# Kernel tuning notes

Measured on AMD Instinct MI355X. Metric: run time of the kernel, lower is better.

Reference implementation:

```python
import jax, jax.numpy as jnp
import numpy as np

N_BASIS = 16


def _kan_layer(x, coeffs, centers):
    # x: [b, in], coeffs: [out, in, n], centers: [n]
    mu = jnp.mean(x, axis=0)
    sd = jnp.std(x, axis=0, ddof=1)  # torch.std is unbiased by default
    xn = jnp.clip((x - mu) / (sd + 1e-6), -3.0, 3.0)
    # Gaussian RBF expansion: [b, in, n]
    basis = jnp.exp(-((xn[..., None] - centers) ** 2) / 0.5)
    return jnp.einsum('bin,oin->bo', basis, coeffs)


def setup_inputs() -> dict:
    key = jax.random.key(0)
    ks = jax.random.split(key, 6)
    B, IN, H = 16384, 256, 512
    return {
        'x': jax.random.normal(ks[0], (B, IN), jnp.float32),
        'coeffs1': jax.random.normal(ks[1], (H, IN, N_BASIS), jnp.float32) * 0.1,
        'coeffs2': jax.random.normal(ks[2], (H, H, N_BASIS), jnp.float32) * 0.1,
        'coeffs3': jax.random.normal(ks[3], (1, H, N_BASIS), jnp.float32) * 0.1,
        'skip_w': jax.random.normal(ks[4], (1, IN), jnp.float32) * 0.05,
        'skip_b': jnp.zeros((1,), jnp.float32),
    }


def reference(x, coeffs1, coeffs2, coeffs3, skip_w, skip_b):
    centers = jnp.linspace(-2.0, 2.0, N_BASIS).astype(x.dtype)
    h = jnp.tanh(_kan_layer(x, coeffs1, centers))
    h = jnp.tanh(_kan_layer(h, coeffs2, centers))
    out = _kan_layer(h, coeffs3, centers)[:, 0]  # squeeze(-1)
    skip = (x @ skip_w.T + skip_b)[:, 0]
    return out + skip
```

## Files before the change

kernel.cpp:

```cpp
#include <hip/hip_runtime.h>
#include <cstdint>
#include <cstddef>

typedef __attribute__((ext_vector_type(8))) _Float16 half8;
typedef __attribute__((ext_vector_type(4))) _Float16 half4;
typedef __attribute__((ext_vector_type(2))) __fp16   fp16x2;
typedef __attribute__((ext_vector_type(4))) float    floatx4;

static constexpr int B_ROWS = 16384;
static constexpr int IN_DIM = 256;
static constexpr int H_DIM  = 512;
static constexpr int NB     = 16;

__device__ __forceinline__ float fast_tanh(float x) {
  float ax = fabsf(x);
  float e  = __expf(2.0f * ax);
  float t  = 1.0f - 2.0f / (e + 1.0f);
  return copysignf(t, x);
}

__device__ __forceinline__ void gld16(const void* g, void* l) {
  __builtin_amdgcn_global_load_lds(
      (const __attribute__((address_space(1))) unsigned int*)g,
      (__attribute__((address_space(3))) unsigned int*)l, 16, 0, 0);
}

__global__ __launch_bounds__(256) void prep_k(const float* __restrict__ c1, _Float16* __restrict__ d1, size_t n41,
                                              const float* __restrict__ c2, _Float16* __restrict__ d2, size_t n42,
                                              const float* __restrict__ X,
                                              float* __restrict__ ps, float* __restrict__ ps2) {
  const int bx = blockIdx.x;
  if (bx < 128) {
    int c     = (bx & 3) * 64 + (threadIdx.x & 63);
    int chunk = threadIdx.x >> 6;
    int seg   = bx >> 2;
    int r0    = seg * 512;
    double s = 0.0, s2 = 0.0;
    for (int r = r0 + chunk; r < r0 + 512; r += 4) {
      float v = X[(size_t)r * IN_DIM + c];
      s += v; s2 += (double)v * (double)v;
    }
    __shared__ float Ls[256], Ls2[256];
    Ls[threadIdx.x] = (float)s; Ls2[threadIdx.x] = (float)s2;
    __syncthreads();
    if (chunk == 0) {
      int cl = threadIdx.x;
      float a  = Ls[cl]  + Ls[cl + 64]  + Ls[cl + 128]  + Ls[cl + 192];
      float b  = Ls2[cl] + Ls2[cl + 64] + Ls2[cl + 128] + Ls2[cl + 192];
      ps [(size_t)seg * IN_DIM + c] = a;
      ps2[(size_t)seg * IN_DIM + c] = b;
    }
  } else {
    size_t tot = n41 + n42;
    int nb_blocks = gridDim.x - 128;
    for (size_t i = (size_t)(bx - 128) * 256 + threadIdx.x; i < tot;
         i += (size_t)nb_blocks * 256) {
      const float4* sp; half4* dp; size_t j;
      if (i < n41) { sp = (const float4*)c1; dp = (half4*)d1; j = i; }
      else         { sp = (const float4*)c2; dp = (half4*)d2; j = i - n41; }
      float4 v = sp[j];
      int nb = (int)((j << 2) & 15);
      half4 r;
      float e0 = -2.f + (float)(nb + 0) * (4.f / 15.f);
      float e1 = -2.f + (float)(nb + 1) * (4.f / 15.f);
      float e2 = -2.f + (float)(nb + 2) * (4.f / 15.f);
      float e3 = -2.f + (float)(nb + 3) * (4.f / 15.f);
      r[0] = (_Float16)(v.x * __expf(-2.f * e0 * e0));
      r[1] = (_Float16)(v.y * __expf(-2.f * e1 * e1));
      r[2] = (_Float16)(v.z * __expf(-2.f * e2 * e2));
      r[3] = (_Float16)(v.w * __expf(-2.f * e3 * e3));
      dp[j] = r;
    }
  }
}

__global__ void stats_final_k(const float* __restrict__ ps,
                              const float* __restrict__ ps2,
                              int segs, int cols, int rows,
                              float* __restrict__ nmi, float* __restrict__ isd,
                              float2* __restrict__ snpk) {
  int c = blockIdx.x * blockDim.x + threadIdx.x;
  if (c >= cols) return;
  double s = 0.0, s2 = 0.0;
  for (int g = 0; g < segs; g++) { s += ps[(size_t)g * cols + c]; s2 += ps2[(size_t)g * cols + c]; }
  double mean = s / rows;
  double var  = (s2 - s * s / rows) / (rows - 1);
  if (var < 0.0) var = 0.0;
  float sd = (float)sqrt(var);
  float iv = 1.0f / (sd + 1e-6f);
  float nm = -(float)mean * iv;
  isd[c] = iv;
  nmi[c] = nm;
  snpk[c] = make_float2(iv, nm);
}

__global__ __launch_bounds__(512, 4) void kan_gemm_fused(const float* __restrict__ X,
                                                         const float2* __restrict__ snpk,
                                                         const _Float16* __restrict__ Bm,
                                                         float* __restrict__ Hout,
                                                         float* __restrict__ psum,
                                                         float* __restrict__ psum2,
                                                         int C) {
  const int K = C << 4;
  const int steps = K >> 6;
  __shared__ __align__(16) unsigned char LDSB[81920];
  _Float16* const Asb = reinterpret_cast<_Float16*>(LDSB);
  _Float16* const Bsb = reinterpret_cast<_Float16*>(LDSB + 32768);
  const int tid  = threadIdx.x;
  const int w = tid >> 6, lane = tid & 63;
  const int wm = w & 1, wn = (w >> 1) & 1, ksw = w >> 2;
  const int lrow = lane & 15, quad = lane >> 4;
  const int row0 = blockIdx.x * 128;
  const int col0 = blockIdx.y * 128;
  const int kq = ksw * 4 + quad;

  const int s_row = tid >> 3;
  const int s_sl  = tid & 7;
  const int s_seg = s_sl ^ ((s_row >> 1) & 7);
  const _Float16* gB = Bm + (size_t)(col0 + s_row) * K + s_seg * 8;

  const int erow = tid & 127;
  const int eh   = tid >> 7;
  const float*  xp  = X    + (size_t)(row0 + erow) * C + eh;
  const float2* snp = snpk + eh;

  floatx4 acc[4][4] = {};

  auto expand_store = [&](float xr, float2 sn, int bufi) {
    float xn = fminf(fmaxf(fmaf(xr, sn.x, sn.y), -3.f), 3.f);
    float Wv = __expf(fmaf(-2.f, xn, -8.f) * xn);
    float g  = __expf((16.f / 15.f) * xn);
    float g2 = g * g, g4 = g2 * g2, g8 = g4 * g4;
    fp16x2 gg = __builtin_amdgcn_cvt_pkrtz(g2, g2);
    union { fp16x2 q[4]; half8 v8; } u0, u1;
    u0.q[0] = __builtin_amdgcn_cvt_pkrtz(Wv, Wv * g);
    u0.q[1] = u0.q[0] * gg;
    u0.q[2] = u0.q[1] * gg;
    u0.q[3] = u0.q[2] * gg;
    float W8 = Wv * g8;
    u1.q[0] = __builtin_amdgcn_cvt_pkrtz(W8, W8 * g);
    u1.q[1] = u1.q[0] * gg;
    u1.q[2] = u1.q[1] * gg;
    u1.q[3] = u1.q[2] * gg;
    int ks0 = 2 * eh;
    *(half8*)&Asb[(size_t)bufi * 8192 + (size_t)(ks0 * 128 + erow) * 8]       = u0.v8;
    *(half8*)&Asb[(size_t)bufi * 8192 + (size_t)((ks0 + 1) * 128 + erow) * 8] = u1.v8;
  };

  float  x0  = xp[0];
  float2 sn0 = snp[0];
  gld16(gB, &Bsb[(size_t)tid * 8]);
  gld16(gB + (size_t)64 * K, &Bsb[(size_t)(tid + 512) * 8]);
  __builtin_amdgcn_sched_barrier(0);
  gld16(gB + 64, &Bsb[8192 + (size_t)tid * 8]);
  gld16(gB + 64 + (size_t)64 * K, &Bsb[8192 + (size_t)(tid + 512) * 8]);
  __builtin_amdgcn_sched_barrier(0);
  float  xv = xp[4];
  float2 sv = snp[4];
  expand_store(x0, sn0, 0);
  asm volatile("s_waitcnt vmcnt(0)" ::: "memory");
  asm volatile("s_waitcnt lgkmcnt(0)" ::: "memory");
  __builtin_amdgcn_s_barrier();
  __builtin_amdgcn_sched_barrier(0);

  int bcur = 0;
  for (int k = 0; k < steps; k++) {
    const int abuf = k & 1;
    const bool more  = (k + 1 < steps);
    const bool more2 = (k + 2 < steps);
    const int b2 = (bcur == 0) ? 2 : bcur - 1;
    if (more2) {
      gld16(gB + (size_t)(k + 2) * 64, &Bsb[(size_t)b2 * 8192 + (size_t)tid * 8]);
      gld16(gB + (size_t)(k + 2) * 64 + (size_t)64 * K,
            &Bsb[(size_t)b2 * 8192 + (size_t)(tid + 512) * 8]);
      __builtin_amdgcn_sched_barrier(0);
    }
    half8 af[4], bf[4];
    auto read_frags = [&]() {
#pragma unroll
      for (int t = 0; t < 4; t++) {
        int arow = wm * 64 + t * 16 + lrow;
        af[t] = *(const half8*)&Asb[(size_t)abuf * 8192 + (size_t)(kq * 128 + arow) * 8];
      }
#pragma unroll
      for (int t = 0; t < 4; t++) {
        int brow = wn * 64 + t * 16 + lrow;
        int bchunk = brow * 8 + (kq ^ ((brow >> 1) & 7));
        bf[t] = *(const half8*)&Bsb[(size_t)bcur * 8192 + (size_t)bchunk * 8];
      }
    };
    auto do_expand = [&]() {
      if (more) {
        expand_store(xv, sv, abuf ^ 1);
        if (more2) {
          xv = xp[4 * (k + 2)];
          sv = snp[4 * (k + 2)];
        }
      }
    };
    if (ksw == 0) {
      read_frags();
      __builtin_amdgcn_s_setprio(1);
#pragma unroll
      for (int tm = 0; tm < 2; tm++)
#pragma unroll
        for (int tn = 0; tn < 4; tn++)
          acc[tm][tn] = __builtin_amdgcn_mfma_f32_16x16x32_f16(af[tm], bf[tn], acc[tm][tn], 0, 0, 0);
      __builtin_amdgcn_s_setprio(0);
      do_expand();
      __builtin_amdgcn_s_setprio(1);
#pragma unroll
      for (int tm = 2; tm < 4; tm++)
#pragma unroll
        for (int tn = 0; tn < 4; tn++)
          acc[tm][tn] = __builtin_amdgcn_mfma_f32_16x16x32_f16(af[tm], bf[tn], acc[tm][tn], 0, 0, 0);
      __builtin_amdgcn_s_setprio(0);
    } else {
      do_expand();
      read_frags();
      __builtin_amdgcn_s_setprio(1);
#pragma unroll
      for (int tm = 0; tm < 4; tm++)
#pragma unroll
        for (int tn = 0; tn < 4; tn++)
          acc[tm][tn] = __builtin_amdgcn_mfma_f32_16x16x32_f16(af[tm], bf[tn], acc[tm][tn], 0, 0, 0);
      __builtin_amdgcn_s_setprio(0);
    }
    asm volatile("s_waitcnt lgkmcnt(0)" ::: "memory");
    __builtin_amdgcn_s_barrier();
    __builtin_amdgcn_sched_barrier(0);
    bcur = (bcur == 2) ? 0 : bcur + 1;
  }

  float* MB = reinterpret_cast<float*>(LDSB);
  const int p = wm * 2 + wn;
  asm volatile("s_waitcnt vmcnt(0)" ::: "memory");
  if (ksw == 1) {
    float* dst = MB + (size_t)p * 4096;
#pragma unroll
    for (int tm = 0; tm < 4; tm++)
#pragma unroll
      for (int tn = 0; tn < 4; tn++)
        *(floatx4*)&dst[((tm * 4 + tn) * 64 + lane) * 4] = acc[tm][tn];
  }
  asm volatile("s_waitcnt lgkmcnt(0)" ::: "memory");
  __builtin_amdgcn_s_barrier();
  __builtin_amdgcn_sched_barrier(0);

  float* Rs1 = MB + 16384;
  float* Rs2 = Rs1 + 256;
  if (ksw == 0) {
    const float* src = MB + (size_t)p * 4096;
    float s1[4] = {0.f, 0.f, 0.f, 0.f}, s2v[4] = {0.f, 0.f, 0.f, 0.f};
#pragma unroll
    for (int tm = 0; tm < 4; tm++) {
#pragma unroll
      for (int tn = 0; tn < 4; tn++) {
        floatx4 other = *(const floatx4*)&src[((tm * 4 + tn) * 64 + lane) * 4];
        int gcol = col0 + wn * 64 + tn * 16 + lrow;
#pragma unroll
        for (int r = 0; r < 4; r++) {
          int grow = row0 + wm * 64 + tm * 16 + quad * 4 + r;
          float v = fast_tanh(acc[tm][tn][r] + other[r]);
          Hout[(size_t)grow * H_DIM + gcol] = v;
          s1[tn] += v; s2v[tn] += v * v;
        }
      }
    }
#pragma unroll
    for (int tn = 0; tn < 4; tn++) {
      s1[tn]  += __shfl_xor(s1[tn], 16);  s1[tn]  += __shfl_xor(s1[tn], 32);
      s2v[tn] += __shfl_xor(s2v[tn], 16); s2v[tn] += __shfl_xor(s2v[tn], 32);
    }
    if (quad == 0) {
#pragma unroll
      for (int tn = 0; tn < 4; tn++) {
        Rs1[wm * 128 + wn * 64 + tn * 16 + lrow] = s1[tn];
        Rs2[wm * 128 + wn * 64 + tn * 16 + lrow] = s2v[tn];
      }
    }
  }
  asm volatile("s_waitcnt lgkmcnt(0)" ::: "memory");
  __builtin_amdgcn_s_barrier();
  __builtin_amdgcn_sched_barrier(0);
  if (tid < 128) {
    psum [(size_t)blockIdx.x * H_DIM + col0 + tid] = Rs1[tid] + Rs1[128 + tid];
    psum2[(size_t)blockIdx.x * H_DIM + col0 + tid] = Rs2[tid] + Rs2[128 + tid];
  }
}

__global__ __launch_bounds__(256) void layer3_k(const float* __restrict__ H2,
                                                const float* __restrict__ nmi,
                                                const float* __restrict__ isd,
                                                const float* __restrict__ C3,
                                                const float* __restrict__ X,
                                                const float* __restrict__ SW,
                                                const float* __restrict__ SB,
                                                float* __restrict__ OUT) {
  int w = threadIdx.x >> 6, lane = threadIdx.x & 63;
  float Kn[NB];
#pragma unroll
  for (int n = 0; n < NB; n++) {
    float c = -2.f + (float)n * (4.f / 15.f);
    Kn[n] = __expf(-2.f * c * c);
  }
  float sb0 = SB[0];
  int row_base = blockIdx.x * 16 + w * 4;
  for (int r = 0; r < 4; r++) {
    int row = row_base + r;
    float s = 0.f;
#pragma unroll
    for (int j = 0; j < 8; j++) {
      int i = lane + 64 * j;
      float hv = H2[(size_t)row * H_DIM + i];
      float xn = fminf(fmaxf(fmaf(hv, isd[i], nmi[i]), -3.f), 3.f);
      float Wf = __expf(fmaf(-2.f, xn, -8.f) * xn);
      float gf = __expf((16.f / 15.f) * xn);
      const floatx4* cp = (const floatx4*)(C3 + (size_t)i * NB);
      floatx4 c0 = cp[0], c1 = cp[1], c2 = cp[2], c3 = cp[3];
      float p = Wf;
#pragma unroll
      for (int n = 0; n < 4; n++) { s += p * Kn[n]      * c0[n]; p *= gf; }
#pragma unroll
      for (int n = 0; n < 4; n++) { s += p * Kn[n + 4]  * c1[n]; p *= gf; }
#pragma unroll
      for (int n = 0; n < 4; n++) { s += p * Kn[n + 8]  * c2[n]; p *= gf; }
#pragma unroll
      for (int n = 0; n < 4; n++) { s += p * Kn[n + 12] * c3[n]; p *= gf; }
    }
#pragma unroll
    for (int j = 0; j < 4; j++) {
      int i = lane + 64 * j;
      s += X[(size_t)row * IN_DIM + i] * SW[i];
    }
#pragma unroll
    for (int off = 32; off > 0; off >>= 1) s += __shfl_down(s, off);
    if (lane == 0) OUT[row] = s + sb0;
  }
}

extern "C" void kernel_launch(void* const* d_in, const int* in_sizes, int n_in,
                              void* d_out, int out_size, void* d_ws, size_t ws_size,
                              hipStream_t stream) {
  const float* x  = (const float*)d_in[0];
  const float* c1 = (const float*)d_in[1];
  const float* c2 = (const float*)d_in[2];
  const float* c3 = (const float*)d_in[3];
  const float* sw = (const float*)d_in[4];
  const float* sb = (const float*)d_in[5];
  float* out = (float*)d_out;

  const int B = B_ROWS, IN = IN_DIM, H = H_DIM;

  char* ws = (char*)d_ws;
  size_t off = 0;
  auto alloc = [&](size_t bytes) -> void* {
    void* p = ws + off;
    off += (bytes + 255) & ~(size_t)255;
    return p;
  };
  _Float16* C1h = (_Float16*)alloc((size_t)H * IN * NB * 2);
  _Float16* C2h = (_Float16*)alloc((size_t)H * H  * NB * 2);
  float* H1 = (float*)alloc((size_t)B * H * 4);
  float* H2 = (float*)alloc((size_t)B * H * 4);
  float* ps  = (float*)alloc(128 * 512 * 4);
  float* ps2 = (float*)alloc(128 * 512 * 4);
  float* nmi = (float*)alloc(512 * 4);
  float* isd = (float*)alloc(512 * 4);
  float2* snpk = (float2*)alloc(512 * 8);

  prep_k<<<128 + 1024, 256, 0, stream>>>(c1, C1h, (size_t)H * IN * NB / 4,
                                         c2, C2h, (size_t)H * H * NB / 4,
                                         x, ps, ps2);
  stats_final_k<<<1, 256, 0, stream>>>(ps, ps2, 32, IN, B, nmi, isd, snpk);

  kan_gemm_fused<<<dim3(B / 128, 4), 512, 0, stream>>>(x, snpk, C1h, H1, ps, ps2, IN);
  stats_final_k<<<2, 256, 0, stream>>>(ps, ps2, 128, H, B, nmi, isd, snpk);

  kan_gemm_fused<<<dim3(B / 128, 4), 512, 0, stream>>>(H1, snpk, C2h, H2, ps, ps2, H);
  stats_final_k<<<2, 256, 0, stream>>>(ps, ps2, 128, H, B, nmi, isd, snpk);

  layer3_k<<<B / 16, 256, 0, stream>>>(H2, nmi, isd, c3, x, sw, sb, out);
}
```

Before: 440.1 us.

## Fuse all stages into one persistent kernel with software grid barriers

The seven separate launches (prep, three column-stat reductions, two GEMM layers, final layer) are merged into one persistent kernel of 512 blocks. The stages are separated by atomic grid barriers in global memory, and the column statistics are finalised in parallel with one column per block. The aim is to remove launch gaps and tail idle time between the dependent stages. In exchange, every block must be co-resident or the barriers deadlock, each barrier adds spin-wait cost, and the barrier counter needs a memset every call.

```diff
diff --git a/kernel.cpp b/kernel.cpp
--- a/kernel.cpp
+++ b/kernel.cpp
@@ -11,6 +11,7 @@
 static constexpr int IN_DIM = 256;
 static constexpr int H_DIM  = 512;
 static constexpr int NB     = 16;
+static constexpr int NBLK   = 512;
 
 __device__ __forceinline__ float fast_tanh(float x) {
   float ax = fabsf(x);
@@ -25,93 +26,59 @@
       (__attribute__((address_space(3))) unsigned int*)l, 16, 0, 0);
 }
 
-__global__ __launch_bounds__(256) void prep_k(const float* __restrict__ c1, _Float16* __restrict__ d1, size_t n41,
-                                              const float* __restrict__ c2, _Float16* __restrict__ d2, size_t n42,
-                                              const float* __restrict__ X,
-                                              float* __restrict__ ps, float* __restrict__ ps2) {
-  const int bx = blockIdx.x;
-  if (bx < 128) {
-    int c     = (bx & 3) * 64 + (threadIdx.x & 63);
-    int chunk = threadIdx.x >> 6;
-    int seg   = bx >> 2;
-    int r0    = seg * 512;
+__device__ __forceinline__ void grid_barrier(unsigned long long* bar, int idx) {
+  __syncthreads();
+  if (threadIdx.x == 0) {
+    __threadfence();
+    __hip_atomic_fetch_add(&bar[idx], 1ull, __ATOMIC_RELEASE, __HIP_MEMORY_SCOPE_AGENT);
+    while (__hip_atomic_load(&bar[idx], __ATOMIC_ACQUIRE, __HIP_MEMORY_SCOPE_AGENT)
+           < (unsigned long long)NBLK) {
+      __builtin_amdgcn_s_sleep(2);
+    }
+    __threadfence();
+  }
+  __syncthreads();
+}
+
+__device__ __forceinline__ void col_stats(const float* ps, const float* ps2,
+                                          int segs, int C, float2* snpk,
+                                          int b, int tid, double* Lred) {
+  if (b < C) {
     double s = 0.0, s2 = 0.0;
-    for (int r = r0 + chunk; r < r0 + 512; r += 4) {
-      float v = X[(size_t)r * IN_DIM + c];
-      s += v; s2 += (double)v * (double)v;
-    }
-    __shared__ float Ls[256], Ls2[256];
-    Ls[threadIdx.x] = (float)s; Ls2[threadIdx.x] = (float)s2;
+    if (tid < segs) {
+      s  = ps [(size_t)tid * C + b];
+      s2 = ps2[(size_t)tid * C + b];
+    }
+    Lred[tid] = s;
+    Lred[512 + tid] = s2;
     __syncthreads();
-    if (chunk == 0) {
-      int cl = threadIdx.x;
-      float a  = Ls[cl]  + Ls[cl + 64]  + Ls[cl + 128]  + Ls[cl + 192];
-      float b  = Ls2[cl] + Ls2[cl + 64] + Ls2[cl + 128] + Ls2[cl + 192];
-      ps [(size_t)seg * IN_DIM + c] = a;
-      ps2[(size_t)seg * IN_DIM + c] = b;
-    }
-  } else {
-    size_t tot = n41 + n42;
-    int nb_blocks = gridDim.x - 128;
-    for (size_t i = (size_t)(bx - 128) * 256 + threadIdx.x; i < tot;
-         i += (size_t)nb_blocks * 256) {
-      const float4* sp; half4* dp; size_t j;
-      if (i < n41) { sp = (const float4*)c1; dp = (half4*)d1; j = i; }
-      else         { sp = (const float4*)c2; dp = (half4*)d2; j = i - n41; }
-      float4 v = sp[j];
-      int nb = (int)((j << 2) & 15);
-      half4 r;
-      float e0 = -2.f + (float)(nb + 0) * (4.f / 15.f);
-      float e1 = -2.f + (float)(nb + 1) * (4.f / 15.f);
-      float e2 = -2.f + (float)(nb + 2) * (4.f / 15.f);
-      float e3 = -2.f + (float)(nb + 3) * (4.f / 15.f);
-      r[0] = (_Float16)(v.x * __expf(-2.f * e0 * e0));
-      r[1] = (_Float16)(v.y * __expf(-2.f * e1 * e1));
-      r[2] = (_Float16)(v.z * __expf(-2.f * e2 * e2));
-      r[3] = (_Float16)(v.w * __expf(-2.f * e3 * e3));
-      dp[j] = r;
-    }
-  }
-}
-
-__global__ void stats_final_k(const float* __restrict__ ps,
-                              const float* __restrict__ ps2,
-                              int segs, int cols, int rows,
-                              float* __restrict__ nmi, float* __restrict__ isd,
-                              float2* __restrict__ snpk) {
-  int c = blockIdx.x * blockDim.x + threadIdx.x;
-  if (c >= cols) return;
-  double s = 0.0, s2 = 0.0;
-  for (int g = 0; g < segs; g++) { s += ps[(size_t)g * cols + c]; s2 += ps2[(size_t)g * cols + c]; }
-  double mean = s / rows;
-  double var  = (s2 - s * s / rows) / (rows - 1);
-  if (var < 0.0) var = 0.0;
-  float sd = (float)sqrt(var);
-  float iv = 1.0f / (sd + 1e-6f);
-  float nm = -(float)mean * iv;
-  isd[c] = iv;
-  nmi[c] = nm;
-  snpk[c] = make_float2(iv, nm);
-}
-
-__global__ __launch_bounds__(512, 4) void kan_gemm_fused(const float* __restrict__ X,
-                                                         const float2* __restrict__ snpk,
-                                                         const _Float16* __restrict__ Bm,
-                                                         float* __restrict__ Hout,
-                                                         float* __restrict__ psum,
-                                                         float* __restrict__ psum2,
-                                                         int C) {
+    if (tid == 0) {
+      double S = 0.0, S2 = 0.0;
+      for (int g = 0; g < segs; g++) { S += Lred[g]; S2 += Lred[512 + g]; }
+      double mean = S / B_ROWS;
+      double var  = (S2 - S * S / B_ROWS) / (B_ROWS - 1);
+      if (var < 0.0) var = 0.0;
+      float iv = 1.0f / ((float)sqrt(var) + 1e-6f);
+      snpk[b] = make_float2(iv, -(float)mean * iv);
+    }
+    __syncthreads();
+  }
+}
+
+__device__ void gemm_phase(const float* __restrict__ X, const float2* __restrict__ snpk,
+                           const _Float16* __restrict__ Bm, float* __restrict__ Hout,
+                           float* __restrict__ psum, float* __restrict__ psum2,
+                           int C, unsigned char* LDSB, int bblk) {
   const int K = C << 4;
   const int steps = K >> 6;
-  __shared__ __align__(16) unsigned char LDSB[81920];
   _Float16* const Asb = reinterpret_cast<_Float16*>(LDSB);
   _Float16* const Bsb = reinterpret_cast<_Float16*>(LDSB + 32768);
   const int tid  = threadIdx.x;
   const int w = tid >> 6, lane = tid & 63;
   const int wm = w & 1, wn = (w >> 1) & 1, ksw = w >> 2;
   const int lrow = lane & 15, quad = lane >> 4;
-  const int row0 = blockIdx.x * 128;
-  const int col0 = blockIdx.y * 128;
+  const int row0 = (bblk & 127) * 128;
+  const int col0 = (bblk >> 7) * 128;
   const int kq = ksw * 4 + quad;
 
   const int s_row = tid >> 3;
@@ -284,58 +251,128 @@
   __builtin_amdgcn_s_barrier();
   __builtin_amdgcn_sched_barrier(0);
   if (tid < 128) {
-    psum [(size_t)blockIdx.x * H_DIM + col0 + tid] = Rs1[tid] + Rs1[128 + tid];
-    psum2[(size_t)blockIdx.x * H_DIM + col0 + tid] = Rs2[tid] + Rs2[128 + tid];
-  }
-}
-
-__global__ __launch_bounds__(256) void layer3_k(const float* __restrict__ H2,
-                                                const float* __restrict__ nmi,
-                                                const float* __restrict__ isd,
-                                                const float* __restrict__ C3,
-                                                const float* __restrict__ X,
-                                                const float* __restrict__ SW,
-                                                const float* __restrict__ SB,
-                                                float* __restrict__ OUT) {
-  int w = threadIdx.x >> 6, lane = threadIdx.x & 63;
-  float Kn[NB];
-#pragma unroll
-  for (int n = 0; n < NB; n++) {
-    float c = -2.f + (float)n * (4.f / 15.f);
-    Kn[n] = __expf(-2.f * c * c);
-  }
-  float sb0 = SB[0];
-  int row_base = blockIdx.x * 16 + w * 4;
-  for (int r = 0; r < 4; r++) {
-    int row = row_base + r;
-    float s = 0.f;
-#pragma unroll
-    for (int j = 0; j < 8; j++) {
-      int i = lane + 64 * j;
-      float hv = H2[(size_t)row * H_DIM + i];
-      float xn = fminf(fmaxf(fmaf(hv, isd[i], nmi[i]), -3.f), 3.f);
-      float Wf = __expf(fmaf(-2.f, xn, -8.f) * xn);
-      float gf = __expf((16.f / 15.f) * xn);
-      const floatx4* cp = (const floatx4*)(C3 + (size_t)i * NB);
-      floatx4 c0 = cp[0], c1 = cp[1], c2 = cp[2], c3 = cp[3];
-      float p = Wf;
-#pragma unroll
-      for (int n = 0; n < 4; n++) { s += p * Kn[n]      * c0[n]; p *= gf; }
-#pragma unroll
-      for (int n = 0; n < 4; n++) { s += p * Kn[n + 4]  * c1[n]; p *= gf; }
-#pragma unroll
-      for (int n = 0; n < 4; n++) { s += p * Kn[n + 8]  * c2[n]; p *= gf; }
-#pragma unroll
-      for (int n = 0; n < 4; n++) { s += p * Kn[n + 12] * c3[n]; p *= gf; }
-    }
-#pragma unroll
-    for (int j = 0; j < 4; j++) {
-      int i = lane + 64 * j;
-      s += X[(size_t)row * IN_DIM + i] * SW[i];
-    }
-#pragma unroll
-    for (int off = 32; off > 0; off >>= 1) s += __shfl_down(s, off);
-    if (lane == 0) OUT[row] = s + sb0;
+    psum [(size_t)(bblk & 127) * H_DIM + col0 + tid] = Rs1[tid] + Rs1[128 + tid];
+    psum2[(size_t)(bblk & 127) * H_DIM + col0 + tid] = Rs2[tid] + Rs2[128 + tid];
+  }
+}
+
+__global__ __launch_bounds__(512, 4) void kan_all(
+    const float* __restrict__ X,  const float* __restrict__ c1,
+    const float* __restrict__ c2, const float* __restrict__ c3,
+    const float* __restrict__ SW, const float* __restrict__ SB,
+    _Float16* __restrict__ C1h, _Float16* __restrict__ C2h,
+    float* __restrict__ H1, float* __restrict__ H2,
+    float* __restrict__ psX, float* __restrict__ ps2X,
+    float* __restrict__ psA, float* __restrict__ ps2A,
+    float* __restrict__ psB, float* __restrict__ ps2B,
+    float2* __restrict__ snpk, unsigned long long* __restrict__ bar,
+    float* __restrict__ OUT) {
+  __shared__ __align__(16) unsigned char LDSB[81920];
+  const int tid = threadIdx.x;
+  const int b   = blockIdx.x;
+  double* Lred = reinterpret_cast<double*>(LDSB);
+
+  {
+    float* Ls  = reinterpret_cast<float*>(LDSB);
+    float* Ls2 = Ls + 512;
+    int lane6 = tid & 63, chunk = tid >> 6;
+    int c  = (b & 3) * 64 + lane6;
+    int sg = b >> 2;
+    int r0 = sg * 128;
+    double s = 0.0, s2 = 0.0;
+    for (int r = r0 + chunk; r < r0 + 128; r += 8) {
+      float v = X[(size_t)r * IN_DIM + c];
+      s += v; s2 += (double)v * (double)v;
+    }
+    Ls[tid] = (float)s; Ls2[tid] = (float)s2;
+    __syncthreads();
+    if (chunk == 0) {
+      float a = 0.f, bb = 0.f;
+#pragma unroll
+      for (int ch = 0; ch < 8; ch++) { a += Ls[lane6 + 64 * ch]; bb += Ls2[lane6 + 64 * ch]; }
+      psX [(size_t)sg * IN_DIM + c] = a;
+      ps2X[(size_t)sg * IN_DIM + c] = bb;
+    }
+    size_t n41 = (size_t)H_DIM * IN_DIM * NB / 4;
+    size_t n42 = (size_t)H_DIM * H_DIM * NB / 4;
+    size_t tot = n41 + n42;
+    for (size_t i = (size_t)b * 512 + tid; i < tot; i += (size_t)NBLK * 512) {
+      const float4* sp; half4* dp; size_t j;
+      if (i < n41) { sp = (const float4*)c1; dp = (half4*)C1h; j = i; }
+      else         { sp = (const float4*)c2; dp = (half4*)C2h; j = i - n41; }
+      float4 v = sp[j];
+      int nb = (int)((j << 2) & 15);
+      half4 r;
+      float e0 = -2.f + (float)(nb + 0) * (4.f / 15.f);
+      float e1 = -2.f + (float)(nb + 1) * (4.f / 15.f);
+      float e2 = -2.f + (float)(nb + 2) * (4.f / 15.f);
+      float e3 = -2.f + (float)(nb + 3) * (4.f / 15.f);
+      r[0] = (_Float16)(v.x * __expf(-2.f * e0 * e0));
+      r[1] = (_Float16)(v.y * __expf(-2.f * e1 * e1));
+      r[2] = (_Float16)(v.z * __expf(-2.f * e2 * e2));
+      r[3] = (_Float16)(v.w * __expf(-2.f * e3 * e3));
+      dp[j] = r;
+    }
+  }
+  grid_barrier(bar, 0);
+
+  col_stats(psX, ps2X, 128, IN_DIM, snpk, b, tid, Lred);
+  grid_barrier(bar, 1);
+
+  gemm_phase(X, snpk, C1h, H1, psA, ps2A, IN_DIM, LDSB, b);
+  grid_barrier(bar, 2);
+
+  col_stats(psA, ps2A, 128, H_DIM, snpk, b, tid, Lred);
+  grid_barrier(bar, 3);
+
+  gemm_phase(H1, snpk, C2h, H2, psB, ps2B, H_DIM, LDSB, b);
+  grid_barrier(bar, 4);
+
+  col_stats(psB, ps2B, 128, H_DIM, snpk, b, tid, Lred);
+  grid_barrier(bar, 5);
+
+  {
+    int w = tid >> 6, lane = tid & 63;
+    float Kn[NB];
+#pragma unroll
+    for (int n = 0; n < NB; n++) {
+      float c = -2.f + (float)n * (4.f / 15.f);
+      Kn[n] = __expf(-2.f * c * c);
+    }
+    float sb0 = SB[0];
+    int row_base = b * 32 + w * 4;
+    for (int r = 0; r < 4; r++) {
+      int row = row_base + r;
+      float s = 0.f;
+#pragma unroll
+      for (int j = 0; j < 8; j++) {
+        int i = lane + 64 * j;
+        float hv = H2[(size_t)row * H_DIM + i];
+        float2 sn = snpk[i];
+        float xn = fminf(fmaxf(fmaf(hv, sn.x, sn.y), -3.f), 3.f);
+        float Wf = __expf(fmaf(-2.f, xn, -8.f) * xn);
+        float gf = __expf((16.f / 15.f) * xn);
+        const floatx4* cp = (const floatx4*)(c3 + (size_t)i * NB);
+        floatx4 c0 = cp[0], c1v = cp[1], c2v = cp[2], c3v = cp[3];
+        float p = Wf;
+#pragma unroll
+        for (int n = 0; n < 4; n++) { s += p * Kn[n]      * c0[n];  p *= gf; }
+#pragma unroll
+        for (int n = 0; n < 4; n++) { s += p * Kn[n + 4]  * c1v[n]; p *= gf; }
+#pragma unroll
+        for (int n = 0; n < 4; n++) { s += p * Kn[n + 8]  * c2v[n]; p *= gf; }
+#pragma unroll
+        for (int n = 0; n < 4; n++) { s += p * Kn[n + 12] * c3v[n]; p *= gf; }
+      }
+#pragma unroll
+      for (int j = 0; j < 4; j++) {
+        int i = lane + 64 * j;
+        s += X[(size_t)row * IN_DIM + i] * SW[i];
+      }
+#pragma unroll
+      for (int off = 32; off > 0; off >>= 1) s += __shfl_down(s, off);
+      if (lane == 0) OUT[row] = s + sb0;
+    }
   }
 }
 
@@ -359,26 +396,23 @@
     off += (bytes + 255) & ~(size_t)255;
     return p;
   };
+  unsigned long long* bar = (unsigned long long*)alloc(256);
   _Float16* C1h = (_Float16*)alloc((size_t)H * IN * NB * 2);
   _Float16* C2h = (_Float16*)alloc((size_t)H * H  * NB * 2);
   float* H1 = (float*)alloc((size_t)B * H * 4);
   float* H2 = (float*)alloc((size_t)B * H * 4);
-  float* ps  = (float*)alloc(128 * 512 * 4);
-  float* ps2 = (float*)alloc(128 * 512 * 4);
-  float* nmi = (float*)alloc(512 * 4);
-  float* isd = (float*)alloc(512 * 4);
+  float* psX  = (float*)alloc(128 * 256 * 4);
+  float* ps2X = (float*)alloc(128 * 256 * 4);
+  float* psA  = (float*)alloc(128 * 512 * 4);
+  float* ps2A = (float*)alloc(128 * 512 * 4);
+  float* psB  = (float*)alloc(128 * 512 * 4);
+  float* ps2B = (float*)alloc(128 * 512 * 4);
   float2* snpk = (float2*)alloc(512 * 8);
 
-  prep_k<<<128 + 1024, 256, 0, stream>>>(c1, C1h, (size_t)H * IN * NB / 4,
-                                         c2, C2h, (size_t)H * H * NB / 4,
-                                         x, ps, ps2);
-  stats_final_k<<<1, 256, 0, stream>>>(ps, ps2, 32, IN, B, nmi, isd, snpk);
-
-  kan_gemm_fused<<<dim3(B / 128, 4), 512, 0, stream>>>(x, snpk, C1h, H1, ps, ps2, IN);
-  stats_final_k<<<2, 256, 0, stream>>>(ps, ps2, 128, H, B, nmi, isd, snpk);
-
-  kan_gemm_fused<<<dim3(B / 128, 4), 512, 0, stream>>>(H1, snpk, C2h, H2, ps, ps2, H);
-  stats_final_k<<<2, 256, 0, stream>>>(ps, ps2, 128, H, B, nmi, isd, snpk);
-
-  layer3_k<<<B / 16, 256, 0, stream>>>(H2, nmi, isd, c3, x, sw, sb, out);
-}
+  hipMemsetAsync(bar, 0, 64, stream);
+
+  kan_all<<<NBLK, 512, 0, stream>>>(x, c1, c2, c3, sw, sb,
+                                    C1h, C2h, H1, H2,
+                                    psX, ps2X, psA, ps2A, psB, ps2B,
+                                    snpk, bar, out);
+}
```

After: 970.8 us. 121% more time.

## Fold column-stats finalization into producer kernels via last-block atomic counters

Applied to the files above, without the earlier changes.

Removes the three separate stats_final_k launches. The last block to finish prep_k and each kan_gemm_fused kernel is detected with an agent-scope atomic counter, and that block reduces the partial sums and writes the packed scale and shift. layer3_k now reads the packed float2 instead of two separate arrays. This cuts launch and dependency gaps between kernels, at the cost of a memset launch, atomics, and a serial reduction tail inside the last block.

```diff
diff --git a/kernel.cpp b/kernel.cpp
--- a/kernel.cpp
+++ b/kernel.cpp
@@ -28,8 +28,12 @@
 __global__ __launch_bounds__(256) void prep_k(const float* __restrict__ c1, _Float16* __restrict__ d1, size_t n41,
                                               const float* __restrict__ c2, _Float16* __restrict__ d2, size_t n42,
                                               const float* __restrict__ X,
-                                              float* __restrict__ ps, float* __restrict__ ps2) {
+                                              float* __restrict__ ps, float* __restrict__ ps2,
+                                              unsigned* __restrict__ cnt,
+                                              float2* __restrict__ snpk) {
   const int bx = blockIdx.x;
+  __shared__ float Ls[256], Ls2[256];
+  __shared__ int lastf;
   if (bx < 128) {
     int c     = (bx & 3) * 64 + (threadIdx.x & 63);
     int chunk = threadIdx.x >> 6;
@@ -40,7 +44,6 @@
       float v = X[(size_t)r * IN_DIM + c];
       s += v; s2 += (double)v * (double)v;
     }
-    __shared__ float Ls[256], Ls2[256];
     Ls[threadIdx.x] = (float)s; Ls2[threadIdx.x] = (float)s2;
     __syncthreads();
     if (chunk == 0) {
@@ -72,26 +75,25 @@
       dp[j] = r;
     }
   }
-}
-
-__global__ void stats_final_k(const float* __restrict__ ps,
-                              const float* __restrict__ ps2,
-                              int segs, int cols, int rows,
-                              float* __restrict__ nmi, float* __restrict__ isd,
-                              float2* __restrict__ snpk) {
-  int c = blockIdx.x * blockDim.x + threadIdx.x;
-  if (c >= cols) return;
-  double s = 0.0, s2 = 0.0;
-  for (int g = 0; g < segs; g++) { s += ps[(size_t)g * cols + c]; s2 += ps2[(size_t)g * cols + c]; }
-  double mean = s / rows;
-  double var  = (s2 - s * s / rows) / (rows - 1);
-  if (var < 0.0) var = 0.0;
-  float sd = (float)sqrt(var);
-  float iv = 1.0f / (sd + 1e-6f);
-  float nm = -(float)mean * iv;
-  isd[c] = iv;
-  nmi[c] = nm;
-  snpk[c] = make_float2(iv, nm);
+  __syncthreads();
+  if (threadIdx.x == 0) {
+    unsigned old = __hip_atomic_fetch_add(cnt, 1u, __ATOMIC_RELEASE, __HIP_MEMORY_SCOPE_AGENT);
+    lastf = (old == gridDim.x - 1) ? 1 : 0;
+  }
+  __syncthreads();
+  if (lastf) {
+    if (threadIdx.x == 0)
+      (void)__hip_atomic_load(cnt, __ATOMIC_ACQUIRE, __HIP_MEMORY_SCOPE_AGENT);
+    __syncthreads();
+    int c = threadIdx.x;
+    double s = 0.0, s2 = 0.0;
+    for (int g = 0; g < 32; g++) { s += ps[(size_t)g * IN_DIM + c]; s2 += ps2[(size_t)g * IN_DIM + c]; }
+    double mean = s / B_ROWS;
+    double var  = (s2 - s * s / B_ROWS) / (B_ROWS - 1);
+    if (var < 0.0) var = 0.0;
+    float iv = 1.0f / ((float)sqrt(var) + 1e-6f);
+    snpk[c] = make_float2(iv, -(float)mean * iv);
+  }
 }
 
 __global__ __launch_bounds__(512, 4) void kan_gemm_fused(const float* __restrict__ X,
@@ -100,7 +102,9 @@
                                                          float* __restrict__ Hout,
                                                          float* __restrict__ psum,
                                                          float* __restrict__ psum2,
-                                                         int C) {
+                                                         int C,
+                                                         unsigned* __restrict__ cnt,
+                                                         float2* __restrict__ snpk_out) {
   const int K = C << 4;
   const int steps = K >> 6;
   __shared__ __align__(16) unsigned char LDSB[81920];
@@ -287,11 +291,33 @@
     psum [(size_t)blockIdx.x * H_DIM + col0 + tid] = Rs1[tid] + Rs1[128 + tid];
     psum2[(size_t)blockIdx.x * H_DIM + col0 + tid] = Rs2[tid] + Rs2[128 + tid];
   }
+
+  int* lastf = reinterpret_cast<int*>(MB + 16896);
+  __syncthreads();
+  if (tid == 0) {
+    unsigned old = __hip_atomic_fetch_add(cnt, 1u, __ATOMIC_RELEASE, __HIP_MEMORY_SCOPE_AGENT);
+    *lastf = (old == gridDim.x * gridDim.y - 1) ? 1 : 0;
+  }
+  __syncthreads();
+  if (*lastf) {
+    if (tid == 0)
+      (void)__hip_atomic_load(cnt, __ATOMIC_ACQUIRE, __HIP_MEMORY_SCOPE_AGENT);
+    __syncthreads();
+    double s = 0.0, s2 = 0.0;
+    for (int g = 0; g < 128; g++) {
+      s  += psum [(size_t)g * H_DIM + tid];
+      s2 += psum2[(size_t)g * H_DIM + tid];
+    }
+    double mean = s / B_ROWS;
+    double var  = (s2 - s * s / B_ROWS) / (B_ROWS - 1);
+    if (var < 0.0) var = 0.0;
+    float iv = 1.0f / ((float)sqrt(var) + 1e-6f);
+    snpk_out[tid] = make_float2(iv, -(float)mean * iv);
+  }
 }
 
 __global__ __launch_bounds__(256) void layer3_k(const float* __restrict__ H2,
-                                                const float* __restrict__ nmi,
-                                                const float* __restrict__ isd,
+                                                const float2* __restrict__ snpk,
                                                 const float* __restrict__ C3,
                                                 const float* __restrict__ X,
                                                 const float* __restrict__ SW,
@@ -313,7 +339,8 @@
     for (int j = 0; j < 8; j++) {
       int i = lane + 64 * j;
       float hv = H2[(size_t)row * H_DIM + i];
-      float xn = fminf(fmaxf(fmaf(hv, isd[i], nmi[i]), -3.f), 3.f);
+      float2 sn = snpk[i];
+      float xn = fminf(fmaxf(fmaf(hv, sn.x, sn.y), -3.f), 3.f);
       float Wf = __expf(fmaf(-2.f, xn, -8.f) * xn);
       float gf = __expf((16.f / 15.f) * xn);
       const floatx4* cp = (const floatx4*)(C3 + (size_t)i * NB);
@@ -359,26 +386,26 @@
     off += (bytes + 255) & ~(size_t)255;
     return p;
   };
+  unsigned* cnts = (unsigned*)alloc(256);
   _Float16* C1h = (_Float16*)alloc((size_t)H * IN * NB * 2);
   _Float16* C2h = (_Float16*)alloc((size_t)H * H  * NB * 2);
   float* H1 = (float*)alloc((size_t)B * H * 4);
   float* H2 = (float*)alloc((size_t)B * H * 4);
   float* ps  = (float*)alloc(128 * 512 * 4);
   float* ps2 = (float*)alloc(128 * 512 * 4);
-  float* nmi = (float*)alloc(512 * 4);
-  float* isd = (float*)alloc(512 * 4);
   float2* snpk = (float2*)alloc(512 * 8);
+
+  hipMemsetAsync(cnts, 0, 256, stream);
 
   prep_k<<<128 + 1024, 256, 0, stream>>>(c1, C1h, (size_t)H * IN * NB / 4,
                                          c2, C2h, (size_t)H * H * NB / 4,
-                                         x, ps, ps2);
-  stats_final_k<<<1, 256, 0, stream>>>(ps, ps2, 32, IN, B, nmi, isd, snpk);
-
-  kan_gemm_fused<<<dim3(B / 128, 4), 512, 0, stream>>>(x, snpk, C1h, H1, ps, ps2, IN);
-  stats_final_k<<<2, 256, 0, stream>>>(ps, ps2, 128, H, B, nmi, isd, snpk);
-
-  kan_gemm_fused<<<dim3(B / 128, 4), 512, 0, stream>>>(H1, snpk, C2h, H2, ps, ps2, H);
-  stats_final_k<<<2, 256, 0, stream>>>(ps, ps2, 128, H, B, nmi, isd, snpk);
-
-  layer3_k<<<B / 16, 256, 0, stream>>>(H2, nmi, isd, c3, x, sw, sb, out);
-}
+                                         x, ps, ps2, cnts + 0, snpk);
+
+  kan_gemm_fused<<<dim3(B / 128, 4), 512, 0, stream>>>(x, snpk, C1h, H1, ps, ps2, IN,
+                                                       cnts + 16, snpk);
+
+  kan_gemm_fused<<<dim3(B / 128, 4), 512, 0, stream>>>(H1, snpk, C2h, H2, ps, ps2, H,
+                                                       cnts + 32, snpk);
+
+  layer3_k<<<B / 16, 256, 0, stream>>>(H2, snpk, c3, x, sw, sb, out);
+}
```

After: 430.3 us. 2.2% less time.
